# Kernel optimization log

Measured on AMD Instinct MI355X. Metric: run time of the kernel, lower is better.

## Reference

```python
import jax, jax.numpy as jnp
import numpy as np

N_NODES = 100000
N_EDGES = 1600000
IN_DIM, HID_DIM, OUT_DIM = 32, 64, 8


def sage_conv(x, src, dst, W_l, b_l, W_r, n_nodes):
    # PyG SAGEConv (aggr='mean', root_weight=True):
    # out_i = W_l @ mean_{j in N(i)} x_j + b_l + W_r @ x_i
    msg_sum = jax.ops.segment_sum(x[src], dst, num_segments=n_nodes)  # [N, F]
    deg = jax.ops.segment_sum(jnp.ones((src.shape[0],), x.dtype), dst,
                              num_segments=n_nodes)  # [N]
    agg = msg_sum / jnp.maximum(deg, 1.0)[:, None]
    return agg @ W_l.T + b_l + x @ W_r.T


def setup_inputs() -> dict:
    key = jax.random.key(0)
    ks = jax.random.split(key, 8)
    x = jax.random.normal(ks[0], (N_NODES, IN_DIM), dtype=jnp.float32)
    edge_index = jax.random.randint(ks[1], (2, N_EDGES), 0, N_NODES, dtype=jnp.int64)
    s1 = 1.0 / np.sqrt(IN_DIM)
    s2 = 1.0 / np.sqrt(HID_DIM)
    return {
        "x": x,
        "edge_index": edge_index,
        "W1_l": jax.random.uniform(ks[2], (HID_DIM, IN_DIM), jnp.float32, -s1, s1),
        "b1": jnp.zeros((HID_DIM,), jnp.float32),
        "W1_r": jax.random.uniform(ks[3], (HID_DIM, IN_DIM), jnp.float32, -s1, s1),
        "W2_l": jax.random.uniform(ks[4], (OUT_DIM, HID_DIM), jnp.float32, -s2, s2),
        "b2": jnp.zeros((OUT_DIM,), jnp.float32),
        "W2_r": jax.random.uniform(ks[5], (OUT_DIM, HID_DIM), jnp.float32, -s2, s2),
    }


def reference(x, edge_index, W1_l, b1, W1_r, W2_l, b2, W2_r):
    src, dst = edge_index[0], edge_index[1]
    h = sage_conv(x, src, dst, W1_l, b1, W1_r, N_NODES)
    h = jax.nn.relu(h)
    out = sage_conv(h, src, dst, W2_l, b2, W2_r, N_NODES)
    return out
```

## Files before the change

### kernel.cpp

```cpp
#include <hip/hip_runtime.h>

#define N_NODES 100000
#define N_EDGES 1600000
#define IN_DIM 32
#define HID_DIM 64
#define OUT_DIM 8
#define CAP 64
#define CHUNK 4096
#define NCHUNK ((N_EDGES + CHUNK - 1) / CHUNK)
#define SLICE_W (N_NODES / 8)

typedef unsigned short u16;
typedef unsigned int u32;
typedef unsigned long long ull;

__device__ __forceinline__ float bf2f(u16 v) {
    return __uint_as_float(((u32)v) << 16);
}

__device__ __forceinline__ u16 f2bf(float f) {
    u32 u = __float_as_uint(f);
    u32 lsb = (u >> 16) & 1u;
    u += 0x7fffu + lsb;
    return (u16)(u >> 16);
}

__device__ __forceinline__ float ldf(const void* p, size_t i, int bf) {
    return bf ? bf2f(((const u16*)p)[i]) : ((const float*)p)[i];
}

__global__ __launch_bounds__(256) void k_prep(
    const int* __restrict__ ei, const u32* __restrict__ xw,
    const void* __restrict__ W1l, const void* __restrict__ b1,
    const void* __restrict__ W1r,
    const void* __restrict__ W2l, const void* __restrict__ b2,
    const void* __restrict__ W2r,
    int* __restrict__ flags,
    float* __restrict__ tW1l, float* __restrict__ tW1r,
    float* __restrict__ tW2l, float* __restrict__ tW2r,
    float* __restrict__ tb1, float* __restrict__ tb2)
{
    __shared__ int bfs;
    int t = threadIdx.x;
    if (t < 64) {
        int v = ei[2 * t + 1];
        ull m1 = __ballot(v == 0);
        u32 w = xw[t];
        u32 b = (w >> 8) & 0x7fu;
        ull m2 = __ballot(b >= 0x38u && b <= 0x41u);
        if (t == 0) {
            flags[0] = (m1 == ~0ULL) ? 1 : 0;
            int bf = (__popcll(m2) >= 56) ? 1 : 0;
            flags[1] = bf;
            bfs = bf;
        }
    }
    __syncthreads();
    int bf = bfs;
    for (int i = t; i < HID_DIM * IN_DIM; i += 256) {
        int o = i / IN_DIM, k = i % IN_DIM;
        tW1l[k * HID_DIM + o] = ldf(W1l, i, bf);
        tW1r[k * HID_DIM + o] = ldf(W1r, i, bf);
    }
    for (int i = t; i < OUT_DIM * HID_DIM; i += 256) {
        int o = i / HID_DIM, k = i % HID_DIM;
        tW2l[k * OUT_DIM + o] = ldf(W2l, i, bf);
        tW2r[k * OUT_DIM + o] = ldf(W2r, i, bf);
    }
    if (t < HID_DIM) tb1[t] = ldf(b1, t, bf);
    if (t < OUT_DIM) tb2[t] = ldf(b2, t, bf);
}

__global__ __launch_bounds__(256) void k_compact(
    const int* __restrict__ ei, const int* __restrict__ flags,
    int* __restrict__ src32, int* __restrict__ dst32)
{
    int e = blockIdx.x * 256 + threadIdx.x;
    if (e >= N_EDGES) return;
    int sh = flags[0];
    size_t off = (size_t)e << sh;
    src32[e] = ei[off];
    dst32[e] = ei[((size_t)N_EDGES << sh) + off];
}

__global__ __launch_bounds__(256) void k_build(
    const int* __restrict__ src32, const int* __restrict__ dst32,
    int* __restrict__ cnt, int* __restrict__ slot)
{
    int slice = blockIdx.x & 7;
    int chunk = blockIdx.x >> 3;
    int lo = slice * SLICE_W, hi = lo + SLICE_W;
    int base = chunk * CHUNK;
    for (int i = threadIdx.x; i < CHUNK; i += 256) {
        int e = base + i;
        if (e >= N_EDGES) break;
        int d = dst32[e];
        if (d < lo || d >= hi) continue;
        int s = src32[e];
        int pos = atomicAdd(&cnt[d], 1);
        if (pos < CAP) slot[(size_t)d * CAP + pos] = s;
    }
}

__global__ __launch_bounds__(256, 8) void k_sage1(
    const void* __restrict__ x, const int* __restrict__ cnt,
    const int* __restrict__ slot,
    const float* __restrict__ tW1l, const float* __restrict__ tW1r,
    const float* __restrict__ tW2l, const float* __restrict__ tW2r,
    const float* __restrict__ tb1, const float* __restrict__ tb2,
    const int* __restrict__ flags,
    float* __restrict__ gbuf, float* __restrict__ rbuf)
{
    __shared__ float aggbuf[8][IN_DIM];
    __shared__ float xbuf[8][IN_DIM];
    __shared__ float hbuf[8][HID_DIM + 1];

    int t = threadIdx.x;
    int bf = flags[1];
    int wid = t >> 6, lane = t & 63;
    int half = lane >> 5;
    int g2 = (lane >> 3) & 3;
    int l = lane & 7;
    int ns = wid * 2 + half;
    int n = blockIdx.x * 8 + ns;
    int deg = cnt[n];
    int cl = (deg < CAP) ? deg : CAP;
    const int* srow = slot + (size_t)n * CAP;

    float a0 = 0, a1 = 0, a2 = 0, a3 = 0;
    float c0 = 0, c1 = 0, c2 = 0, c3 = 0;
    int j = g2;
    for (; j + 4 < cl; j += 8) {
        int sA = srow[j];
        int sB = srow[j + 4];
        if (bf) {
            ushort4 vA = reinterpret_cast<const ushort4*>((const u16*)x + (size_t)sA * IN_DIM)[l];
            ushort4 vB = reinterpret_cast<const ushort4*>((const u16*)x + (size_t)sB * IN_DIM)[l];
            a0 += bf2f(vA.x); a1 += bf2f(vA.y); a2 += bf2f(vA.z); a3 += bf2f(vA.w);
            c0 += bf2f(vB.x); c1 += bf2f(vB.y); c2 += bf2f(vB.z); c3 += bf2f(vB.w);
        } else {
            float4 vA = reinterpret_cast<const float4*>((const float*)x + (size_t)sA * IN_DIM)[l];
            float4 vB = reinterpret_cast<const float4*>((const float*)x + (size_t)sB * IN_DIM)[l];
            a0 += vA.x; a1 += vA.y; a2 += vA.z; a3 += vA.w;
            c0 += vB.x; c1 += vB.y; c2 += vB.z; c3 += vB.w;
        }
    }
    if (j < cl) {
        int s = srow[j];
        if (bf) {
            ushort4 v = reinterpret_cast<const ushort4*>((const u16*)x + (size_t)s * IN_DIM)[l];
            a0 += bf2f(v.x); a1 += bf2f(v.y); a2 += bf2f(v.z); a3 += bf2f(v.w);
        } else {
            float4 v = reinterpret_cast<const float4*>((const float*)x + (size_t)s * IN_DIM)[l];
            a0 += v.x; a1 += v.y; a2 += v.z; a3 += v.w;
        }
    }
    a0 += c0; a1 += c1; a2 += c2; a3 += c3;
    a0 += __shfl_xor(a0, 8, 64);  a0 += __shfl_xor(a0, 16, 64);
    a1 += __shfl_xor(a1, 8, 64);  a1 += __shfl_xor(a1, 16, 64);
    a2 += __shfl_xor(a2, 8, 64);  a2 += __shfl_xor(a2, 16, 64);
    a3 += __shfl_xor(a3, 8, 64);  a3 += __shfl_xor(a3, 16, 64);
    if (g2 == 0) {
        aggbuf[ns][4 * l + 0] = a0; aggbuf[ns][4 * l + 1] = a1;
        aggbuf[ns][4 * l + 2] = a2; aggbuf[ns][4 * l + 3] = a3;
    } else if (g2 == 1) {
        float f0, f1, f2, f3;
        if (bf) {
            ushort4 v = reinterpret_cast<const ushort4*>((const u16*)x + (size_t)n * IN_DIM)[l];
            f0 = bf2f(v.x); f1 = bf2f(v.y); f2 = bf2f(v.z); f3 = bf2f(v.w);
        } else {
            float4 v = reinterpret_cast<const float4*>((const float*)x + (size_t)n * IN_DIM)[l];
            f0 = v.x; f1 = v.y; f2 = v.z; f3 = v.w;
        }
        xbuf[ns][4 * l + 0] = f0; xbuf[ns][4 * l + 1] = f1;
        xbuf[ns][4 * l + 2] = f2; xbuf[ns][4 * l + 3] = f3;
    }
    __syncthreads();

    float rd0 = 1.0f / fmaxf((float)__shfl(deg, 0, 64), 1.0f);
    float rd1 = 1.0f / fmaxf((float)__shfl(deg, 32, 64), 1.0f);
    int s0 = wid * 2, s1 = wid * 2 + 1;
    int o = lane;
    float bb = tb1[o];
    float acc0 = bb, acc1 = bb;
    #pragma unroll 8
    for (int k = 0; k < IN_DIM; k++) {
        float wl = tW1l[k * HID_DIM + o];
        float wr = tW1r[k * HID_DIM + o];
        acc0 += (aggbuf[s0][k] * rd0) * wl + xbuf[s0][k] * wr;
        acc1 += (aggbuf[s1][k] * rd1) * wl + xbuf[s1][k] * wr;
    }
    hbuf[s0][o] = fmaxf(acc0, 0.0f);
    hbuf[s1][o] = fmaxf(acc1, 0.0f);
    __syncthreads();

    float ga = 0.0f, ra = 0.0f;
    #pragma unroll 4
    for (int m = 0; m < 16; m++) {
        int k = g2 * 16 + m;
        float hv = hbuf[ns][k];
        ga += hv * tW2l[k * OUT_DIM + l];
        ra += hv * tW2r[k * OUT_DIM + l];
    }
    ga += __shfl_xor(ga, 8, 64);  ga += __shfl_xor(ga, 16, 64);
    ra += __shfl_xor(ra, 8, 64);  ra += __shfl_xor(ra, 16, 64);
    if (g2 == 0) {
        gbuf[(size_t)n * OUT_DIM + l] = ga;
        rbuf[(size_t)n * OUT_DIM + l] = ra + tb2[l];
    }
}

__global__ __launch_bounds__(256) void k_sage3(
    const float* __restrict__ gbuf, const float* __restrict__ rbuf,
    const int* __restrict__ cnt, const int* __restrict__ slot,
    const int* __restrict__ flags, void* __restrict__ out)
{
    int t = threadIdx.x;
    int grp = t >> 3, l = t & 7;
    int n = blockIdx.x * 32 + grp;
    int deg = cnt[n];
    int cl = (deg < CAP) ? deg : CAP;
    const int* srow = slot + (size_t)n * CAP;
    float a0 = 0.0f, a1 = 0.0f;
    int j = 0;
    for (; j + 1 < cl; j += 2) {
        int v0 = srow[j];
        int v1 = srow[j + 1];
        a0 += gbuf[(size_t)v0 * OUT_DIM + l];
        a1 += gbuf[(size_t)v1 * OUT_DIM + l];
    }
    if (j < cl) a0 += gbuf[(size_t)srow[j] * OUT_DIM + l];
    float res = (a0 + a1) / fmaxf((float)deg, 1.0f) + rbuf[(size_t)n * OUT_DIM + l];
    size_t oi = (size_t)n * OUT_DIM + l;
    if (flags[1]) ((u16*)out)[oi] = f2bf(res);
    else          ((float*)out)[oi] = res;
}

extern "C" void kernel_launch(void* const* d_in, const int* in_sizes, int n_in,
                              void* d_out, int out_size, void* d_ws, size_t ws_size,
                              hipStream_t stream) {
    const void* x   = d_in[0];
    const int*  ei  = (const int*)d_in[1];
    const void* W1l = d_in[2];
    const void* b1  = d_in[3];
    const void* W1r = d_in[4];
    const void* W2l = d_in[5];
    const void* b2  = d_in[6];
    const void* W2r = d_in[7];

    int* flags   = (int*)d_ws;
    int* cnt     = flags + 4;
    float* tW1l  = (float*)(cnt + N_NODES);
    float* tW1r  = tW1l + IN_DIM * HID_DIM;
    float* tW2l  = tW1r + IN_DIM * HID_DIM;
    float* tW2r  = tW2l + HID_DIM * OUT_DIM;
    float* tb1   = tW2r + HID_DIM * OUT_DIM;
    float* tb2   = tb1 + HID_DIM;
    int* slot    = (int*)(tb2 + OUT_DIM);
    float* gbuf  = (float*)(slot + (size_t)N_NODES * CAP);
    float* rbuf  = gbuf + (size_t)N_NODES * OUT_DIM;
    int* src32   = (int*)(rbuf + (size_t)N_NODES * OUT_DIM);
    int* dst32   = src32 + N_EDGES;

    hipMemsetAsync(d_ws, 0, (size_t)(4 + N_NODES) * sizeof(int), stream);

    k_prep<<<1, 256, 0, stream>>>(ei, (const u32*)x, W1l, b1, W1r, W2l, b2, W2r,
                                  flags, tW1l, tW1r, tW2l, tW2r, tb1, tb2);
    k_compact<<<(N_EDGES + 255) / 256, 256, 0, stream>>>(ei, flags, src32, dst32);
    k_build<<<NCHUNK * 8, 256, 0, stream>>>(src32, dst32, cnt, slot);
    k_sage1<<<N_NODES / 8, 256, 0, stream>>>(x, cnt, slot, tW1l, tW1r,
                                             tW2l, tW2r, tb1, tb2, flags, gbuf, rbuf);
    k_sage3<<<N_NODES / 32, 256, 0, stream>>>(gbuf, rbuf, cnt, slot, flags, d_out);
}
```

Measured before the change: 264.5 us.

## Replace compact+sliced build with radix partition of edges by destination slice

Swaps the compaction kernel and the 8x-redundant sliced scan of all edges for a partition kernel. It reads each edge once, histograms destinations into 8 slices, and writes packed (src<<14 | local dst) words into per-slice queues. A second kernel then drains each slice queue to fill the CSR-like slot table with atomics. This removes the repeated full reads of the dst array and the separate int32 copies. The cost is extra shared-memory atomics and the risk of overflowing the fixed queue capacity or the 14-bit local index field.

```diff
diff --git a/kernel.cpp b/kernel.cpp
--- a/kernel.cpp
+++ b/kernel.cpp
@@ -9,6 +9,7 @@
 #define CHUNK 4096
 #define NCHUNK ((N_EDGES + CHUNK - 1) / CHUNK)
 #define SLICE_W (N_NODES / 8)
+#define QCAP 262144
 
 typedef unsigned short u16;
 typedef unsigned int u32;
@@ -71,32 +72,64 @@
     if (t < OUT_DIM) tb2[t] = ldf(b2, t, bf);
 }
 
-__global__ __launch_bounds__(256) void k_compact(
+__global__ __launch_bounds__(256) void k_part(
     const int* __restrict__ ei, const int* __restrict__ flags,
-    int* __restrict__ src32, int* __restrict__ dst32)
-{
-    int e = blockIdx.x * 256 + threadIdx.x;
-    if (e >= N_EDGES) return;
+    int* __restrict__ qcnt, u32* __restrict__ qbuf)
+{
+    __shared__ int hist[4][8], wbase[4][8], lcur[4][8], gbase[8];
+    int t = threadIdx.x, w = t >> 6;
+    if (t < 32) { hist[t >> 3][t & 7] = 0; lcur[t >> 3][t & 7] = 0; }
+    __syncthreads();
     int sh = flags[0];
-    size_t off = (size_t)e << sh;
-    src32[e] = ei[off];
-    dst32[e] = ei[((size_t)N_EDGES << sh) + off];
-}
-
-__global__ __launch_bounds__(256) void k_build(
-    const int* __restrict__ src32, const int* __restrict__ dst32,
+    int e0 = blockIdx.x * CHUNK;
+    int myd[16], mys[16];
+    #pragma unroll
+    for (int i = 0; i < 16; i++) {
+        int e = e0 + i * 256 + t;
+        if (e < N_EDGES) {
+            size_t off = (size_t)e << sh;
+            mys[i] = ei[off];
+            int d = ei[((size_t)N_EDGES << sh) + off];
+            myd[i] = d;
+            atomicAdd(&hist[w][d / SLICE_W], 1);
+        } else myd[i] = -1;
+    }
+    __syncthreads();
+    if (t < 8) {
+        int tot = hist[0][t] + hist[1][t] + hist[2][t] + hist[3][t];
+        gbase[t] = atomicAdd(&qcnt[t], tot);
+    }
+    __syncthreads();
+    if (t < 32) {
+        int w2 = t >> 3, s = t & 7;
+        int p = gbase[s];
+        for (int w3 = 0; w3 < w2; w3++) p += hist[w3][s];
+        wbase[w2][s] = p;
+    }
+    __syncthreads();
+    #pragma unroll
+    for (int i = 0; i < 16; i++) {
+        int d = myd[i];
+        if (d >= 0) {
+            int s = d / SLICE_W;
+            int p = wbase[w][s] + atomicAdd(&lcur[w][s], 1);
+            qbuf[(size_t)s * QCAP + p] = ((u32)mys[i] << 14) | (u32)(d - s * SLICE_W);
+        }
+    }
+}
+
+__global__ __launch_bounds__(256) void k_build2(
+    const int* __restrict__ qcnt, const u32* __restrict__ qbuf,
     int* __restrict__ cnt, int* __restrict__ slot)
 {
-    int slice = blockIdx.x & 7;
-    int chunk = blockIdx.x >> 3;
-    int lo = slice * SLICE_W, hi = lo + SLICE_W;
-    int base = chunk * CHUNK;
-    for (int i = threadIdx.x; i < CHUNK; i += 256) {
-        int e = base + i;
-        if (e >= N_EDGES) break;
-        int d = dst32[e];
-        if (d < lo || d >= hi) continue;
-        int s = src32[e];
+    int slice = blockIdx.x & 7, bi = blockIdx.x >> 3;
+    int m = qcnt[slice];
+    int lo = slice * SLICE_W;
+    const u32* q = qbuf + (size_t)slice * QCAP;
+    for (int i = bi * 256 + threadIdx.x; i < m; i += 64 * 256) {
+        u32 u = q[i];
+        int d = lo + (int)(u & 0x3FFFu);
+        int s = (int)(u >> 14);
         int pos = atomicAdd(&cnt[d], 1);
         if (pos < CAP) slot[(size_t)d * CAP + pos] = s;
     }
@@ -250,24 +283,24 @@
 
     int* flags   = (int*)d_ws;
     int* cnt     = flags + 4;
-    float* tW1l  = (float*)(cnt + N_NODES);
+    int* qcnt    = cnt + N_NODES;
+    float* tW1l  = (float*)(qcnt + 8);
     float* tW1r  = tW1l + IN_DIM * HID_DIM;
     float* tW2l  = tW1r + IN_DIM * HID_DIM;
     float* tW2r  = tW2l + HID_DIM * OUT_DIM;
     float* tb1   = tW2r + HID_DIM * OUT_DIM;
     float* tb2   = tb1 + HID_DIM;
     int* slot    = (int*)(tb2 + OUT_DIM);
-    float* gbuf  = (float*)(slot + (size_t)N_NODES * CAP);
+    u32* qbuf    = (u32*)(slot + (size_t)N_NODES * CAP);
+    float* gbuf  = (float*)(qbuf + (size_t)8 * QCAP);
     float* rbuf  = gbuf + (size_t)N_NODES * OUT_DIM;
-    int* src32   = (int*)(rbuf + (size_t)N_NODES * OUT_DIM);
-    int* dst32   = src32 + N_EDGES;
-
-    hipMemsetAsync(d_ws, 0, (size_t)(4 + N_NODES) * sizeof(int), stream);
+
+    hipMemsetAsync(d_ws, 0, (size_t)(4 + N_NODES + 8) * sizeof(int), stream);
 
     k_prep<<<1, 256, 0, stream>>>(ei, (const u32*)x, W1l, b1, W1r, W2l, b2, W2r,
                                   flags, tW1l, tW1r, tW2l, tW2r, tb1, tb2);
-    k_compact<<<(N_EDGES + 255) / 256, 256, 0, stream>>>(ei, flags, src32, dst32);
-    k_build<<<NCHUNK * 8, 256, 0, stream>>>(src32, dst32, cnt, slot);
+    k_part<<<NCHUNK, 256, 0, stream>>>(ei, flags, qcnt, qbuf);
+    k_build2<<<512, 256, 0, stream>>>(qcnt, qbuf, cnt, slot);
     k_sage1<<<N_NODES / 8, 256, 0, stream>>>(x, cnt, slot, tW1l, tW1r,
                                              tW2l, tW2r, tb1, tb2, flags, gbuf, rbuf);
     k_sage3<<<N_NODES / 32, 256, 0, stream>>>(gbuf, rbuf, cnt, slot, flags, d_out);
```

New measurement: 265.4 us. No clear change (+0.3%).
